# Performance work log

Hardware: AMD Instinct MI355X
Metric: run time of the kernel (lower is better)

Reference implementation:

```python
import jax, jax.numpy as jnp
import numpy as np

B, N, P, C, H = 8, 512, 16, 512, 8
HD = C // H  # 64


def setup_inputs() -> dict:
    key = jax.random.key(0)
    k1, k2, k3, k4, k5 = jax.random.split(key, 5)
    x = jax.random.normal(k1, (B, N, P, C), dtype=jnp.float32)
    # binary observation mask; force slot 0 valid so masked mean never divides by 0
    mask = (jax.random.uniform(k2, (B, N, P)) > 0.3).astype(jnp.float32)
    mask = mask.at[:, :, 0].set(1.0)
    lens = jax.random.randint(k3, (B,), 1, N)
    lens_mask = jnp.ones((B, N), dtype=jnp.float32)
    # parameters (torch Linear stored as [in, out] here; qkv_bias=False, proj has bias)
    Wqkv = jax.random.normal(k4, (C, 3 * C), dtype=jnp.float32) * (1.0 / np.sqrt(C))
    Wproj = jax.random.normal(k5, (C, C), dtype=jnp.float32) * (1.0 / np.sqrt(C))
    bproj = jnp.zeros((C,), dtype=jnp.float32)
    return {"x": x, "mask": mask, "lens": lens, "lens_mask": lens_mask,
            "Wqkv": Wqkv, "Wproj": Wproj, "bproj": bproj}


def reference(x, mask, lens, lens_mask, Wqkv, Wproj, bproj):
    # lens / lens_mask are unused by the original forward
    b, n, p, c = x.shape
    h, hd = H, c // H
    qkv = jnp.einsum('bnpc,cd->bnpd', x, Wqkv).reshape(b, n, p, 3, h, hd)
    # q: take P-slot 0                       -> [B,H,N,hd]
    q = qkv[:, :, 0, 0].transpose(0, 2, 1, 3)
    # k: masked mean over P                  -> [B,H,N,hd]
    m = mask[..., None, None]                      # [B,N,P,1,1]
    k = (jnp.where(m > 0, qkv[:, :, :, 1], 0.0).sum(axis=2) / m.sum(axis=2))
    k = k.transpose(0, 2, 1, 3)
    # v: pack P into channel dim             -> [B,H,N,hd*P]
    v = qkv[:, :, :, 2].transpose(0, 3, 1, 4, 2).reshape(b, h, n, hd * p)
    # SDPA over N (scale by 1/sqrt(head_dim of q))
    scale = 1.0 / np.sqrt(hd)
    attn = jax.nn.softmax(jnp.einsum('bhnd,bhmd->bhnm', q, k) * scale, axis=-1)
    out = jnp.einsum('bhnm,bhme->bhne', attn, v)            # [B,H,N,hd*P]
    # unpack P back out                       -> [B,N,P,C]
    out = out.reshape(b, h, n, hd, p).transpose(0, 2, 4, 1, 3).reshape(b, n, p, c)
    return out @ Wproj + bproj
```

## Files before the change

### kernel.cpp

```cpp
#include <hip/hip_runtime.h>

typedef _Float16 f16;
typedef __attribute__((ext_vector_type(8))) _Float16 half8;
typedef __attribute__((ext_vector_type(2))) _Float16 half2v;
typedef __attribute__((ext_vector_type(4))) float float4v;

#define MODE_QK 0
#define MODE_V 1
#define MODE_PV 2
#define MODE_PROJ 3


__device__ __forceinline__ void gload16(const f16* g, f16* l) {
    __builtin_amdgcn_global_load_lds(
        (const __attribute__((address_space(1))) void*)g,
        (__attribute__((address_space(3))) void*)l, 16, 0, 0);
}

__global__ __launch_bounds__(256) void prep_kernel(
    const float* __restrict__ x, const float* __restrict__ mask,
    const float* __restrict__ Wqkv, const float* __restrict__ Wproj,
    f16* __restrict__ xf, f16* __restrict__ xmean,
    f16* __restrict__ WT, f16* __restrict__ WpT)
{
    if (blockIdx.x >= 4096) {
        int idx = (blockIdx.x - 4096) * 256 + threadIdx.x;
        if (idx < 1536 * 512) {
            int d = idx >> 9, c = idx & 511;
            WT[idx] = (f16)Wqkv[c * 1536 + d];
        } else {
            int i2 = idx - 1536 * 512;
            int d = i2 >> 9, c = i2 & 511;
            WpT[i2] = (f16)Wproj[c * 512 + d];
        }
        return;
    }
    int bn = blockIdx.x;
    int t = threadIdx.x;
    const float* xrow = x + (size_t)bn * 16 * 512;
    const float* mrow = mask + (size_t)bn * 16;
    float msum = 0.f;
    #pragma unroll
    for (int p = 0; p < 16; p++) msum += mrow[p];
    int c = t * 2;
    float a0 = 0.f, a1 = 0.f;
    #pragma unroll
    for (int p = 0; p < 16; p++) {
        float2 v = *(const float2*)(xrow + p * 512 + c);
        float m = mrow[p];
        a0 += m * v.x; a1 += m * v.y;
        half2v h; h[0] = (f16)v.x; h[1] = (f16)v.y;
        *(half2v*)(xf + (size_t)bn * 16 * 512 + p * 512 + c) = h;
    }
    float inv = 1.f / msum;
    half2v hm; hm[0] = (f16)(a0 * inv); hm[1] = (f16)(a1 * inv);
    *(half2v*)(xmean + (size_t)bn * 512 + c) = hm;
}

template<int MODE, int NXB, int NYB>
__global__ __launch_bounds__(256) void gemm128(
    const f16* __restrict__ pA, const f16* __restrict__ pA2,
    const f16* __restrict__ pB,
    f16* __restrict__ outa, f16* __restrict__ outb,
    float* __restrict__ outf, const float* __restrict__ bias)
{
    __shared__ __align__(16) f16 sm[24576];
    const int t = threadIdx.x;
    const int lane = t & 63;
    const int w = t >> 6;
    const int wm = w & 1, wn = w >> 1;
    const int quad = lane >> 4, l15 = lane & 15;

    const int chunk = (int)gridDim.x >> 3;
    const int L = ((int)blockIdx.x & 7) * chunk + ((int)blockIdx.x >> 3);
    const int xb = L & ((1 << NXB) - 1);
    const int rest = L >> NXB;
    const int yb = rest & ((1 << NYB) - 1);
    const int z = rest >> NYB;
    const int n0 = xb * 128;
    const int m0 = yb * 128;
    int vb = 0, vp = 0;

    const f16* Abase; size_t sA;
    const f16* Bbase; size_t sB;
    if constexpr (MODE == MODE_QK) {
        if (n0 < 512) { Abase = pA;  sA = 8192; }
        else          { Abase = pA2; sA = 512;  }
        Bbase = pB; sB = 512;
    } else if constexpr (MODE == MODE_V) {
        vb = z >> 4; vp = z & 15;
        Abase = pA; sA = 512;
        Bbase = pB + ((size_t)vb * 512 * 16 + vp) * 512; sB = 8192;
    } else if constexpr (MODE == MODE_PV) {
        Abase = pA + (size_t)z * 512 * 512; sA = 512;
        Bbase = pB + (size_t)z * 1024 * 512; sB = 512;
    } else {
        Abase = pA; sA = 512;
        Bbase = pB; sB = 512;
    }

    const int rlo = (lane >> 2);
    const int kof = (((lane & 3) ^ ((rlo >> 1) & 3)) * 8);
    const f16* ga0 = Abase + (size_t)(m0 + w * 16 + rlo) * sA + kof;
    const f16* ga1 = Abase + (size_t)(m0 + (w + 4) * 16 + rlo) * sA + kof;
    const f16* gb0 = Bbase + (size_t)(n0 + w * 16 + rlo) * sB + kof;
    const f16* gb1 = Bbase + (size_t)(n0 + (w + 4) * 16 + rlo) * sB + kof;

    float4v acc[4][4];
    #pragma unroll
    for (int i = 0; i < 4; i++)
        #pragma unroll
        for (int j = 0; j < 4; j++)
            acc[i][j] = (float4v){0.f, 0.f, 0.f, 0.f};

    const int sws = (l15 >> 1) & 3;

#define STAGE(dst)                                                     \
    do {                                                               \
        f16* d_ = (dst);                                               \
        gload16(ga0, d_ + w * 512); gload16(ga1, d_ + (w + 4) * 512);  \
        gload16(gb0, d_ + 4096 + w * 512);                             \
        gload16(gb1, d_ + 4096 + (w + 4) * 512);                       \
        ga0 += 32; ga1 += 32; gb0 += 32; gb1 += 32;                    \
    } while (0)

#define COMPUTE(buf)                                                         \
    do {                                                                     \
        const f16* Asr_ = (buf);                                             \
        const f16* Bsr_ = Asr_ + 4096;                                       \
        half8 af[4], bf[4];                                                  \
        _Pragma("unroll")                                                    \
        for (int mi = 0; mi < 4; mi++)                                       \
            af[mi] = *(const half8*)&Asr_[(wm * 64 + mi * 16 + l15) * 32 +   \
                                          ((quad ^ sws) * 8)];               \
        _Pragma("unroll")                                                    \
        for (int ni = 0; ni < 4; ni++)                                       \
            bf[ni] = *(const half8*)&Bsr_[(wn * 64 + ni * 16 + l15) * 32 +   \
                                          ((quad ^ sws) * 8)];               \
        _Pragma("unroll")                                                    \
        for (int mi = 0; mi < 4; mi++)                                       \
            _Pragma("unroll")                                                \
            for (int ni = 0; ni < 4; ni++)                                   \
                acc[mi][ni] = __builtin_amdgcn_mfma_f32_16x16x32_f16(        \
                    af[mi], bf[ni], acc[mi][ni], 0, 0, 0);                   \
    } while (0)

    f16* pc = sm;
    f16* pn = sm + 8192;
    f16* pf = sm + 16384;
    STAGE(pc);
    STAGE(pn);
    for (int kt = 0; kt < 14; kt++) {
        asm volatile("s_waitcnt vmcnt(4)" ::: "memory");
        __builtin_amdgcn_s_barrier();
        __builtin_amdgcn_sched_barrier(0);
        STAGE(pf);
        COMPUTE(pc);
        f16* tmp = pc; pc = pn; pn = pf; pf = tmp;
    }
    asm volatile("s_waitcnt vmcnt(4)" ::: "memory");
    __builtin_amdgcn_s_barrier();
    __builtin_amdgcn_sched_barrier(0);
    COMPUTE(pc);
    { f16* tmp = pc; pc = pn; pn = pf; pf = tmp; }
    asm volatile("s_waitcnt vmcnt(0)" ::: "memory");
    __builtin_amdgcn_s_barrier();
    __builtin_amdgcn_sched_barrier(0);
    COMPUTE(pc);
#undef STAGE
#undef COMPUTE

    __syncthreads();

    if constexpr (MODE == MODE_PROJ) {
        float* pwf = (float*)sm + w * 1088;
        const int rr4 = lane >> 4, c4c = (lane & 15) * 4;
        float4v bb = *(const float4v*)&bias[n0 + wn * 64 + c4c];
        #pragma unroll
        for (int mi = 0; mi < 4; mi++) {
            #pragma unroll
            for (int ni = 0; ni < 4; ni++)
                #pragma unroll
                for (int i = 0; i < 4; i++)
                    pwf[(quad * 4 + i) * 68 + ni * 16 + l15] = acc[mi][ni][i];
            #pragma unroll
            for (int s = 0; s < 4; s++) {
                int r = s * 4 + rr4;
                float4v v = *(const float4v*)&pwf[r * 68 + c4c];
                *(float4v*)&outf[(size_t)(m0 + wm * 64 + mi * 16 + r) * 512 +
                                 n0 + wn * 64 + c4c] = v + bb;
            }
        }
    } else {
        f16* pw = sm + w * 2304;
        const int rr8 = lane >> 3, c8 = (lane & 7) * 8;
        #pragma unroll
        for (int hf = 0; hf < 2; hf++) {
            #pragma unroll
            for (int mh = 0; mh < 2; mh++) {
                int mi = hf * 2 + mh;
                #pragma unroll
                for (int ni = 0; ni < 4; ni++)
                    #pragma unroll
                    for (int i = 0; i < 4; i++)
                        pw[(mh * 16 + quad * 4 + i) * 72 + ni * 16 + l15] =
                            (f16)acc[mi][ni][i];
            }
            #pragma unroll
            for (int s = 0; s < 4; s++) {
                int r = s * 8 + rr8;
                half8 v = *(const half8*)&pw[r * 72 + c8];
                int gr = m0 + wm * 64 + hf * 32 + r;
                int gc = n0 + wn * 64 + c8;
                if constexpr (MODE == MODE_QK) {
                    int b = gr >> 9, n = gr & 511;
                    if (gc < 512)
                        *(half8*)&outa[(((size_t)(b * 8 + (gc >> 6))) * 512 + n) * 64 + (gc & 63)] = v;
                    else {
                        int jj = gc - 512;
                        *(half8*)&outb[(((size_t)(b * 8 + (jj >> 6))) * 512 + n) * 64 + (jj & 63)] = v;
                    }
                } else if constexpr (MODE == MODE_V) {
                    int h = gr >> 6, dd = gr & 63;
                    *(half8*)&outa[(((size_t)(vb * 8 + h)) * 1024 + vp * 64 + dd) * 512 + gc] = v;
                } else {
                    int p = gc >> 6, dd = gc & 63;
                    int b = z >> 3, h = z & 7;
                    *(half8*)&outa[((size_t)(b * 512 + gr) * 16 + p) * 512 + h * 64 + dd] = v;
                }
            }
        }
    }
}

__global__ __launch_bounds__(256) void qk_softmax_kernel(
    const f16* __restrict__ q, const f16* __restrict__ k, f16* __restrict__ Pout)
{
    __shared__ __align__(16) f16 sm[32768];
    const int t = threadIdx.x;
    const int lane = t & 63, w = t >> 6;
    const int quad = lane >> 4, l15 = lane & 15;
    const int L = ((int)blockIdx.x & 7) * 64 + ((int)blockIdx.x >> 3);
    const int bh = L >> 3;
    const int n0 = (L & 7) * 64;

    const f16* kbase = k + (size_t)bh * 512 * 64;

    #pragma unroll
    for (int i = 0; i < 16; i++) {
        int cid = i * 256 + t;
        int row = cid >> 3, off = cid & 7;
        gload16(kbase + row * 64 + ((off ^ (row & 7)) << 3),
                sm + i * 2048 + w * 512 + (lane & 63) * 8);
    }
    const f16* qp = q + ((size_t)bh * 512 + n0 + w * 16 + l15) * 64 + quad * 8;
    half8 a0 = *(const half8*)qp;
    half8 a1 = *(const half8*)(qp + 32);

    asm volatile("s_waitcnt vmcnt(0)" ::: "memory");
    __builtin_amdgcn_s_barrier();
    __builtin_amdgcn_sched_barrier(0);

    float4v acc[32];
    #pragma unroll
    for (int f = 0; f < 32; f++) acc[f] = (float4v){0.f, 0.f, 0.f, 0.f};
    #pragma unroll
    for (int fl = 0; fl < 32; fl++) {
        int row16 = fl * 16 + l15;
        int sw = row16 & 7;
        half8 b0 = *(const half8*)&sm[row16 * 64 + ((quad ^ sw) << 3)];
        half8 b1 = *(const half8*)&sm[row16 * 64 + (((quad + 4) ^ sw) << 3)];
        acc[fl] = __builtin_amdgcn_mfma_f32_16x16x32_f16(a0, b0, acc[fl], 0, 0, 0);
        acc[fl] = __builtin_amdgcn_mfma_f32_16x16x32_f16(a1, b1, acc[fl], 0, 0, 0);
    }

    float mx0 = -3e38f, mx1 = -3e38f, mx2 = -3e38f, mx3 = -3e38f;
    #pragma unroll
    for (int f = 0; f < 32; f++) {
        mx0 = fmaxf(mx0, acc[f][0]); mx1 = fmaxf(mx1, acc[f][1]);
        mx2 = fmaxf(mx2, acc[f][2]); mx3 = fmaxf(mx3, acc[f][3]);
    }
    #pragma unroll
    for (int off = 1; off < 16; off <<= 1) {
        mx0 = fmaxf(mx0, __shfl_xor(mx0, off));
        mx1 = fmaxf(mx1, __shfl_xor(mx1, off));
        mx2 = fmaxf(mx2, __shfl_xor(mx2, off));
        mx3 = fmaxf(mx3, __shfl_xor(mx3, off));
    }
    float s0 = 0.f, s1 = 0.f, s2 = 0.f, s3 = 0.f;
    #pragma unroll
    for (int f = 0; f < 32; f++) {
        float e0 = __expf(0.125f * (acc[f][0] - mx0));
        float e1 = __expf(0.125f * (acc[f][1] - mx1));
        float e2 = __expf(0.125f * (acc[f][2] - mx2));
        float e3 = __expf(0.125f * (acc[f][3] - mx3));
        acc[f][0] = e0; acc[f][1] = e1; acc[f][2] = e2; acc[f][3] = e3;
        s0 += e0; s1 += e1; s2 += e2; s3 += e3;
    }
    #pragma unroll
    for (int off = 1; off < 16; off <<= 1) {
        s0 += __shfl_xor(s0, off);
        s1 += __shfl_xor(s1, off);
        s2 += __shfl_xor(s2, off);
        s3 += __shfl_xor(s3, off);
    }
    float r0 = 1.f / s0, r1 = 1.f / s1, r2 = 1.f / s2, r3 = 1.f / s3;

    __syncthreads();
    f16* pb = sm + w * 4224;
    const int rr = lane >> 2, cb = (lane & 3) * 64;
    #pragma unroll
    for (int cc = 0; cc < 2; cc++) {
        #pragma unroll
        for (int ff = 0; ff < 16; ff++) {
            int f = cc * 16 + ff;
            pb[(quad * 4 + 0) * 264 + ff * 16 + l15] = (f16)(acc[f][0] * r0);
            pb[(quad * 4 + 1) * 264 + ff * 16 + l15] = (f16)(acc[f][1] * r1);
            pb[(quad * 4 + 2) * 264 + ff * 16 + l15] = (f16)(acc[f][2] * r2);
            pb[(quad * 4 + 3) * 264 + ff * 16 + l15] = (f16)(acc[f][3] * r3);
        }
        size_t gb = ((size_t)bh * 512 + n0 + w * 16 + rr) * 512 + cc * 256 + cb;
        #pragma unroll
        for (int s = 0; s < 8; s++) {
            half8 v = *(const half8*)&pb[rr * 264 + cb + s * 8];
            *(half8*)&Pout[gb + s * 8] = v;
        }
    }
}

extern "C" void kernel_launch(void* const* d_in, const int* in_sizes, int n_in,
                              void* d_out, int out_size, void* d_ws, size_t ws_size,
                              hipStream_t stream)
{
    (void)in_sizes; (void)n_in; (void)out_size; (void)ws_size;
    const float* x     = (const float*)d_in[0];
    const float* mask  = (const float*)d_in[1];
    const float* Wqkv  = (const float*)d_in[4];
    const float* Wproj = (const float*)d_in[5];
    const float* bproj = (const float*)d_in[6];
    float* out = (float*)d_out;
    char* ws = (char*)d_ws;

    f16* xf16  = (f16*)(ws + 0);
    f16* vT    = (f16*)(ws + 67108864);
    f16* xmean = (f16*)(ws + 134217728);
    f16* WT    = (f16*)(ws + 138412032);
    f16* WpT   = (f16*)(ws + 139984896);
    f16* qb    = (f16*)(ws + 140509184);
    f16* kb    = (f16*)(ws + 144703488);
    f16* Pm    = (f16*)(ws + 148897792);
    f16* ypre  = xf16;

    prep_kernel<<<dim3(8192), dim3(256), 0, stream>>>(
        x, mask, Wqkv, Wproj, xf16, xmean, WT, WpT);
    gemm128<MODE_QK, 3, 5><<<dim3(256), dim3(256), 0, stream>>>(
        xf16, xmean, WT, qb, kb, nullptr, nullptr);
    gemm128<MODE_V, 2, 2><<<dim3(2048), dim3(256), 0, stream>>>(
        WT + 1024 * 512, nullptr, xf16, vT, nullptr, nullptr, nullptr);
    qk_softmax_kernel<<<dim3(512), dim3(256), 0, stream>>>(qb, kb, Pm);
    gemm128<MODE_PV, 3, 2><<<dim3(2048), dim3(256), 0, stream>>>(
        Pm, nullptr, vT, ypre, nullptr, nullptr, nullptr);
    gemm128<MODE_PROJ, 2, 9><<<dim3(2048), dim3(256), 0, stream>>>(
        ypre, nullptr, WpT, nullptr, nullptr, out, bproj);
}
```

Baseline: 405.3 us.

## Fuse QK softmax with PV matmul, keeping probabilities in LDS

```diff
diff --git a/kernel.cpp b/kernel.cpp
--- a/kernel.cpp
+++ b/kernel.cpp
@@ -91,9 +91,6 @@
         vb = z >> 4; vp = z & 15;
         Abase = pA; sA = 512;
         Bbase = pB + ((size_t)vb * 512 * 16 + vp) * 512; sB = 8192;
-    } else if constexpr (MODE == MODE_PV) {
-        Abase = pA + (size_t)z * 512 * 512; sA = 512;
-        Bbase = pB + (size_t)z * 1024 * 512; sB = 512;
     } else {
         Abase = pA; sA = 512;
         Bbase = pB; sB = 512;
@@ -220,23 +217,20 @@
                         int jj = gc - 512;
                         *(half8*)&outb[(((size_t)(b * 8 + (jj >> 6))) * 512 + n) * 64 + (jj & 63)] = v;
                     }
-                } else if constexpr (MODE == MODE_V) {
+                } else {
                     int h = gr >> 6, dd = gr & 63;
                     *(half8*)&outa[(((size_t)(vb * 8 + h)) * 1024 + vp * 64 + dd) * 512 + gc] = v;
-                } else {
-                    int p = gc >> 6, dd = gc & 63;
-                    int b = z >> 3, h = z & 7;
-                    *(half8*)&outa[((size_t)(b * 512 + gr) * 16 + p) * 512 + h * 64 + dd] = v;
                 }
             }
         }
     }
 }
 
-__global__ __launch_bounds__(256) void qk_softmax_kernel(
-    const f16* __restrict__ q, const f16* __restrict__ k, f16* __restrict__ Pout)
+__global__ __launch_bounds__(256) void attn_pv_kernel(
+    const f16* __restrict__ q, const f16* __restrict__ k,
+    const f16* __restrict__ vT, f16* __restrict__ ypre)
 {
-    __shared__ __align__(16) f16 sm[32768];
+    __shared__ __align__(16) f16 sm[37376];
     const int t = threadIdx.x;
     const int lane = t & 63, w = t >> 6;
     const int quad = lane >> 4, l15 = lane & 15;
@@ -245,13 +239,12 @@
     const int n0 = (L & 7) * 64;
 
     const f16* kbase = k + (size_t)bh * 512 * 64;
-
     #pragma unroll
     for (int i = 0; i < 16; i++) {
         int cid = i * 256 + t;
         int row = cid >> 3, off = cid & 7;
         gload16(kbase + row * 64 + ((off ^ (row & 7)) << 3),
-                sm + i * 2048 + w * 512 + (lane & 63) * 8);
+                sm + i * 2048 + w * 512 + lane * 8);
     }
     const f16* qp = q + ((size_t)bh * 512 + n0 + w * 16 + l15) * 64 + quad * 8;
     half8 a0 = *(const half8*)qp;
@@ -304,26 +297,78 @@
         s2 += __shfl_xor(s2, off);
         s3 += __shfl_xor(s3, off);
     }
-    float r0 = 1.f / s0, r1 = 1.f / s1, r2 = 1.f / s2, r3 = 1.f / s3;
+    float rr[4];
+    rr[0] = 1.f / s0; rr[1] = 1.f / s1; rr[2] = 1.f / s2; rr[3] = 1.f / s3;
 
     __syncthreads();
-    f16* pb = sm + w * 4224;
-    const int rr = lane >> 2, cb = (lane & 3) * 64;
-    #pragma unroll
-    for (int cc = 0; cc < 2; cc++) {
-        #pragma unroll
-        for (int ff = 0; ff < 16; ff++) {
-            int f = cc * 16 + ff;
-            pb[(quad * 4 + 0) * 264 + ff * 16 + l15] = (f16)(acc[f][0] * r0);
-            pb[(quad * 4 + 1) * 264 + ff * 16 + l15] = (f16)(acc[f][1] * r1);
-            pb[(quad * 4 + 2) * 264 + ff * 16 + l15] = (f16)(acc[f][2] * r2);
-            pb[(quad * 4 + 3) * 264 + ff * 16 + l15] = (f16)(acc[f][3] * r3);
-        }
-        size_t gb = ((size_t)bh * 512 + n0 + w * 16 + rr) * 512 + cc * 256 + cb;
-        #pragma unroll
-        for (int s = 0; s < 8; s++) {
-            half8 v = *(const half8*)&pb[rr * 264 + cb + s * 8];
-            *(half8*)&Pout[gb + s * 8] = v;
+    {
+        const int prow_b = w * 16 + quad * 4;
+        #pragma unroll
+        for (int f = 0; f < 32; f++) {
+            #pragma unroll
+            for (int i = 0; i < 4; i++) {
+                int row = prow_b + i;
+                int col = f * 16 + l15;
+                int slot = (col >> 3) ^ ((row ^ (row >> 3)) & 7);
+                sm[row * 512 + slot * 8 + (col & 7)] = (f16)(acc[f][i] * rr[i]);
+            }
+        }
+    }
+    __syncthreads();
+
+    const int swA = (l15 ^ (l15 >> 3)) & 7;
+    const f16* vbase = vT + (size_t)bh * 1024 * 512;
+    const int b_ = bh >> 3, h_ = bh & 7;
+    f16* pw = sm + 32768 + w * 1152;
+    for (int ec = 0; ec < 4; ec++) {
+        const f16* vb = vbase + (size_t)(ec * 256 + w * 64) * 512;
+        float4v acc2[4][4];
+        #pragma unroll
+        for (int mi = 0; mi < 4; mi++)
+            #pragma unroll
+            for (int nf = 0; nf < 4; nf++)
+                acc2[mi][nf] = (float4v){0.f, 0.f, 0.f, 0.f};
+        half8 bc[4], bn_[4];
+        #pragma unroll
+        for (int nf = 0; nf < 4; nf++)
+            bc[nf] = *(const half8*)&vb[(size_t)(nf * 16 + l15) * 512 + quad * 8];
+        #pragma unroll
+        for (int ks = 0; ks < 16; ks++) {
+            if (ks < 15) {
+                #pragma unroll
+                for (int nf = 0; nf < 4; nf++)
+                    bn_[nf] = *(const half8*)&vb[(size_t)(nf * 16 + l15) * 512 +
+                                                 (ks + 1) * 32 + quad * 8];
+            }
+            half8 af[4];
+            #pragma unroll
+            for (int mi = 0; mi < 4; mi++)
+                af[mi] = *(const half8*)&sm[(mi * 16 + l15) * 512 +
+                                            (((ks * 4 + quad) ^ swA ^ (mi << 1)) << 3)];
+            #pragma unroll
+            for (int mi = 0; mi < 4; mi++)
+                #pragma unroll
+                for (int nf = 0; nf < 4; nf++)
+                    acc2[mi][nf] = __builtin_amdgcn_mfma_f32_16x16x32_f16(
+                        af[mi], bc[nf], acc2[mi][nf], 0, 0, 0);
+            #pragma unroll
+            for (int nf = 0; nf < 4; nf++) bc[nf] = bn_[nf];
+        }
+        const int p_of = ec * 4 + w;
+        const int r = lane >> 2, c16 = (lane & 3) * 16;
+        #pragma unroll
+        for (int mi = 0; mi < 4; mi++) {
+            #pragma unroll
+            for (int nf = 0; nf < 4; nf++)
+                #pragma unroll
+                for (int i = 0; i < 4; i++)
+                    pw[(quad * 4 + i) * 72 + nf * 16 + l15] = (f16)acc2[mi][nf][i];
+            int n_ = n0 + mi * 16 + r;
+            size_t gb = ((size_t)(b_ * 512 + n_) * 16 + p_of) * 512 + h_ * 64 + c16;
+            half8 v0 = *(const half8*)&pw[r * 72 + c16];
+            half8 v1 = *(const half8*)&pw[r * 72 + c16 + 8];
+            *(half8*)&ypre[gb] = v0;
+            *(half8*)&ypre[gb + 8] = v1;
         }
     }
 }
@@ -348,7 +393,6 @@
     f16* WpT   = (f16*)(ws + 139984896);
     f16* qb    = (f16*)(ws + 140509184);
     f16* kb    = (f16*)(ws + 144703488);
-    f16* Pm    = (f16*)(ws + 148897792);
     f16* ypre  = xf16;
 
     prep_kernel<<<dim3(8192), dim3(256), 0, stream>>>(
@@ -357,9 +401,7 @@
         xf16, xmean, WT, qb, kb, nullptr, nullptr);
     gemm128<MODE_V, 2, 2><<<dim3(2048), dim3(256), 0, stream>>>(
         WT + 1024 * 512, nullptr, xf16, vT, nullptr, nullptr, nullptr);
-    qk_softmax_kernel<<<dim3(512), dim3(256), 0, stream>>>(qb, kb, Pm);
-    gemm128<MODE_PV, 3, 2><<<dim3(2048), dim3(256), 0, stream>>>(
-        Pm, nullptr, vT, ypre, nullptr, nullptr, nullptr);
+    attn_pv_kernel<<<dim3(512), dim3(256), 0, stream>>>(qb, kb, vT, ypre);
     gemm128<MODE_PROJ, 2, 9><<<dim3(2048), dim3(256), 0, stream>>>(
         ypre, nullptr, WpT, nullptr, nullptr, out, bproj);
 }
```

Measured after the change: 462.3 us. +14.1%, slower.
